# Kernel optimization log

Hardware: AMD Instinct MI355X
Metric: run time of the kernel (lower is better)

## Reference

```python
import jax, jax.numpy as jnp
import numpy as np

B, D, H = 65536, 32, 128


def setup_inputs() -> dict:
    key = jax.random.key(0)
    ks = jax.random.split(key, 6)
    return {
        "x": jax.random.normal(ks[0], (B, 1, D), dtype=jnp.float32),
        "W1": jax.random.normal(ks[1], (D, H), dtype=jnp.float32) * (1.0 / np.sqrt(D)),
        "b1": jax.random.normal(ks[2], (H,), dtype=jnp.float32) * 0.01,
        "W2": jax.random.normal(ks[3], (H, D), dtype=jnp.float32) * (1.0 / np.sqrt(H)),
        "b2": jax.random.normal(ks[4], (D,), dtype=jnp.float32) * 0.01,
        "theta_0": jnp.array([0.5], dtype=jnp.float32),
    }


def reference(x, W1, b1, W2, b2, theta_0):
    # x: (B, 1, D). Network u: D -> H -> D with tanh (transformation=none, no bounds).
    xf = x[:, 0, :]  # (B, D)

    def u_fn(xv):  # (D,) -> (D,)
        h = jnp.tanh(xv @ W1 + b1)
        return h @ W2 + b2

    # div u = trace of per-sample Jacobian, computed in ONE vectorized forward-mode
    # sweep (replaces the per-dimension torch.autograd.grad loop).
    div_u = jax.vmap(lambda xv: jnp.trace(jax.jacfwd(u_fn)(xv)))(xf)  # (B,)

    u_x = jax.vmap(u_fn)(xf)  # (B, D)
    grad_log_pi = -xf  # standard normal: grad log pi(x) = -x, shape (B, D)
    grad_log_pi_u = jnp.sum(grad_log_pi * u_x, axis=-1)  # (B,)  == (B,1,D)@(B,D,1) flattened

    out = (grad_log_pi_u + div_u + theta_0)[:, None]  # (B, 1)
    return out
```

## Files before the change

### kernel.cpp

```cpp
#include <hip/hip_runtime.h>


#define NROWS 65536
#define DD 32
#define HH 128
#define NTILE 25

typedef __attribute__((ext_vector_type(8))) short short8;
typedef __attribute__((ext_vector_type(4))) float f32x4;

static __device__ __forceinline__ unsigned short f2bf(float f) {
    unsigned u = __float_as_uint(f);
    u += 0x7fff + ((u >> 16) & 1);
    return (unsigned short)(u >> 16);
}
static __device__ __forceinline__ float bf2f(unsigned short h) {
    return __uint_as_float(((unsigned)h) << 16);
}

__global__ __launch_bounds__(256) void stein_pack(
    const float* __restrict__ W1, const float* __restrict__ W2,
    const float* __restrict__ b2, unsigned short* __restrict__ packed,
    float* __restrict__ c) {
    const int blk = blockIdx.x;
    if (blk < NTILE) {
        for (int idx = threadIdx.x; idx < 512; idx += 256) {
            const int l = idx >> 3, j = idx & 7;
            const int k = (l >> 4) * 8 + j;
            const int cc = l & 15;
            unsigned short val;
            if (blk < 8) {
                val = f2bf(W1[k * HH + blk * 16 + cc]);
            } else if (blk < 16) {
                float w = W1[k * HH + (blk - 8) * 16 + cc];
                val = f2bf(w - bf2f(f2bf(w)));
            } else {
                const int n = (blk - 16) * 16 + cc;
                float w = (n < HH) ? W2[n * DD + k] : ((n == HH) ? b2[k] : 0.f);
                val = f2bf(w);
            }
            packed[blk * 512 + idx] = val;
        }
    } else {
        const int k = threadIdx.x;
        if (k < HH) {
            float acc = 0.f;
#pragma unroll
            for (int i = 0; i < DD; ++i)
                acc = fmaf(W1[i * HH + k], W2[k * DD + i], acc);
            c[k] = acc;
        }
    }
}

__global__ __launch_bounds__(256) void stein_main(
    const float* __restrict__ x, const float* __restrict__ b1,
    const float* __restrict__ theta, const unsigned short* __restrict__ packed,
    const float* __restrict__ c, float* __restrict__ out) {
    __shared__ unsigned short lb[NTILE * 512];

    {
        const float4* src = (const float4*)packed;
        float4* dst = (float4*)lb;
        for (int i = threadIdx.x; i < NTILE * 512 / 8; i += 256) dst[i] = src[i];
    }
    __syncthreads();

    const int lane = threadIdx.x & 63;
    const int wv = threadIdx.x >> 6;
    const int quad = lane >> 4;
    const int cl = lane & 15;
    const int rowbase = blockIdx.x * 64 + wv * 16;

    const float* xr = x + (size_t)(rowbase + cl) * DD + quad * 8;
    const float4 x0 = *(const float4*)xr;
    const float4 x1 = *(const float4*)(xr + 4);
    const float xv[8] = {x0.x, x0.y, x0.z, x0.w, x1.x, x1.y, x1.z, x1.w};
    short8 aHi, aLo;
#pragma unroll
    for (int j = 0; j < 8; ++j) {
        const unsigned short h = f2bf(xv[j]);
        aHi[j] = (short)h;
        aLo[j] = (short)f2bf(xv[j] - bf2f(h));
    }

    float ckv[8], b1v[8];
#pragma unroll
    for (int t = 0; t < 8; ++t) {
        ckv[t] = c[t * 16 + cl];
        b1v[t] = b1[t * 16 + cl];
    }

    const f32x4 zero = {0.f, 0.f, 0.f, 0.f};
    float sa[4] = {0.f, 0.f, 0.f, 0.f};

#pragma unroll
    for (int t = 0; t < 8; ++t) {
        const short8 bH = *(const short8*)(lb + t * 512 + lane * 8);
        const short8 bL = *(const short8*)(lb + (8 + t) * 512 + lane * 8);
        const short8 bW = *(const short8*)(lb + (16 + t) * 512 + lane * 8);
        f32x4 z = zero;
        z = __builtin_amdgcn_mfma_f32_16x16x32_bf16(aLo, bH, z, 0, 0, 0);
        z = __builtin_amdgcn_mfma_f32_16x16x32_bf16(aHi, bL, z, 0, 0, 0);
        z = __builtin_amdgcn_mfma_f32_16x16x32_bf16(aHi, bH, z, 0, 0, 0);
        const f32x4 v = __builtin_amdgcn_mfma_f32_16x16x32_bf16(aHi, bW, zero, 0, 0, 0);
#pragma unroll
        for (int r = 0; r < 4; ++r) {
            float zz = z[r] + b1v[t];
            zz = fminf(fmaxf(zz, -15.f), 15.f);
            const float e = __expf(2.f * zz);
            const float h = fmaf(-2.f, __builtin_amdgcn_rcpf(e + 1.f), 1.f);
            const float ck = ckv[t];
            sa[r] += ck - h * fmaf(h, ck, v[r]);
        }
    }
    {
        const short8 bW = *(const short8*)(lb + 24 * 512 + lane * 8);
        const f32x4 v = __builtin_amdgcn_mfma_f32_16x16x32_bf16(aHi, bW, zero, 0, 0, 0);
#pragma unroll
        for (int r = 0; r < 4; ++r) sa[r] -= v[r];
    }

#pragma unroll
    for (int r = 0; r < 4; ++r) {
#pragma unroll
        for (int m = 1; m < 16; m <<= 1) sa[r] += __shfl_xor(sa[r], m, 64);
    }

    if (cl == 0) {
        const float th = theta[0];
        float4 o;
        o.x = sa[0] + th;
        o.y = sa[1] + th;
        o.z = sa[2] + th;
        o.w = sa[3] + th;
        *(float4*)(out + rowbase + quad * 4) = o;
    }
}

extern "C" void kernel_launch(void* const* d_in, const int* in_sizes, int n_in,
                              void* d_out, int out_size, void* d_ws, size_t ws_size,
                              hipStream_t stream) {
    const float* x = (const float*)d_in[0];
    const float* W1 = (const float*)d_in[1];
    const float* b1 = (const float*)d_in[2];
    const float* W2 = (const float*)d_in[3];
    const float* b2 = (const float*)d_in[4];
    const float* theta = (const float*)d_in[5];
    float* out = (float*)d_out;

    unsigned short* packed = (unsigned short*)d_ws;
    float* c = (float*)((char*)d_ws + NTILE * 512 * 2);

    stein_pack<<<NTILE + 1, 256, 0, stream>>>(W1, W2, b2, packed, c);
    stein_main<<<NROWS / 64, 256, 0, stream>>>(x, b1, theta, packed, c, out);
}
```

Baseline: 73.51 us.

## Fuse weight packing into main kernel and process 128 rows per block

Removes the separate packing kernel and its workspace round trip. Each block now converts W1, W2 and b2 to split-bf16 tiles in shared memory and computes the W1·W2 diagonal itself, using 512 threads that each cover 16 rows per wave. It also drops the tanh input clamp and moves c and b1 from registers to shared-memory reads. In exchange, every block repeats the weight conversion from L2, and relying on exp overflowing to inf without the clamp is a small numerical risk.

```diff
diff --git a/kernel.cpp b/kernel.cpp
--- a/kernel.cpp
+++ b/kernel.cpp
@@ -18,63 +18,84 @@
     return __uint_as_float(((unsigned)h) << 16);
 }
 
-__global__ __launch_bounds__(256) void stein_pack(
-    const float* __restrict__ W1, const float* __restrict__ W2,
-    const float* __restrict__ b2, unsigned short* __restrict__ packed,
-    float* __restrict__ c) {
-    const int blk = blockIdx.x;
-    if (blk < NTILE) {
-        for (int idx = threadIdx.x; idx < 512; idx += 256) {
-            const int l = idx >> 3, j = idx & 7;
-            const int k = (l >> 4) * 8 + j;
-            const int cc = l & 15;
-            unsigned short val;
-            if (blk < 8) {
-                val = f2bf(W1[k * HH + blk * 16 + cc]);
-            } else if (blk < 16) {
-                float w = W1[k * HH + (blk - 8) * 16 + cc];
-                val = f2bf(w - bf2f(f2bf(w)));
-            } else {
-                const int n = (blk - 16) * 16 + cc;
-                float w = (n < HH) ? W2[n * DD + k] : ((n == HH) ? b2[k] : 0.f);
-                val = f2bf(w);
-            }
-            packed[blk * 512 + idx] = val;
-        }
-    } else {
-        const int k = threadIdx.x;
-        if (k < HH) {
-            float acc = 0.f;
-#pragma unroll
-            for (int i = 0; i < DD; ++i)
-                acc = fmaf(W1[i * HH + k], W2[k * DD + i], acc);
-            c[k] = acc;
-        }
-    }
-}
+__global__ __launch_bounds__(512, 4) void stein_fused(
+    const float* __restrict__ x, const float* __restrict__ W1,
+    const float* __restrict__ b1, const float* __restrict__ W2,
+    const float* __restrict__ b2, const float* __restrict__ theta,
+    float* __restrict__ out) {
+    __shared__ unsigned short lb[NTILE * 512];
+    __shared__ float cs[HH];
+    __shared__ float b1s[HH];
 
-__global__ __launch_bounds__(256) void stein_main(
-    const float* __restrict__ x, const float* __restrict__ b1,
-    const float* __restrict__ theta, const unsigned short* __restrict__ packed,
-    const float* __restrict__ c, float* __restrict__ out) {
-    __shared__ unsigned short lb[NTILE * 512];
-
-    {
-        const float4* src = (const float4*)packed;
-        float4* dst = (float4*)lb;
-        for (int i = threadIdx.x; i < NTILE * 512 / 8; i += 256) dst[i] = src[i];
-    }
-    __syncthreads();
-
-    const int lane = threadIdx.x & 63;
-    const int wv = threadIdx.x >> 6;
+    const int tid = threadIdx.x;
+    const int lane = tid & 63;
+    const int wv = tid >> 6;
     const int quad = lane >> 4;
     const int cl = lane & 15;
-    const int rowbase = blockIdx.x * 64 + wv * 16;
+    const int rowbase = blockIdx.x * 128 + wv * 16;
 
     const float* xr = x + (size_t)(rowbase + cl) * DD + quad * 8;
     const float4 x0 = *(const float4*)xr;
     const float4 x1 = *(const float4*)(xr + 4);
+
+    if (tid < 256) {
+        const int n = tid & 127;
+        const int half = tid >> 7;
+        const int t = n >> 4, cc = n & 15;
+#pragma unroll
+        for (int g = 0; g < 2; ++g) {
+            const int kg = half * 2 + g;
+            short8 hi, lo;
+#pragma unroll
+            for (int j = 0; j < 8; ++j) {
+                const float w = W1[(kg * 8 + j) * HH + n];
+                const unsigned short h = f2bf(w);
+                hi[j] = (short)h;
+                lo[j] = (short)f2bf(w - bf2f(h));
+            }
+            *(short8*)(lb + t * 512 + (kg * 16 + cc) * 8) = hi;
+            *(short8*)(lb + (8 + t) * 512 + (kg * 16 + cc) * 8) = lo;
+        }
+    } else if (tid < 384) {
+        const int n = tid - 256;
+        const int t2 = 16 + (n >> 4), cc = n & 15;
+        float row[32];
+        const float4* wr = (const float4*)(W2 + n * DD);
+#pragma unroll
+        for (int q = 0; q < 8; ++q) {
+            const float4 f = wr[q];
+            row[4 * q + 0] = f.x;
+            row[4 * q + 1] = f.y;
+            row[4 * q + 2] = f.z;
+            row[4 * q + 3] = f.w;
+        }
+        float acc = 0.f;
+#pragma unroll
+        for (int k = 0; k < 32; ++k) acc = fmaf(W1[k * HH + n], row[k], acc);
+        cs[n] = acc;
+#pragma unroll
+        for (int g = 0; g < 4; ++g) {
+            short8 v;
+#pragma unroll
+            for (int j = 0; j < 8; ++j) v[j] = (short)f2bf(row[g * 8 + j]);
+            *(short8*)(lb + t2 * 512 + (g * 16 + cc) * 8) = v;
+        }
+    } else {
+        const int u = tid - 384;
+        if (u < 16) {
+#pragma unroll
+            for (int g = 0; g < 4; ++g) {
+                short8 v;
+#pragma unroll
+                for (int j = 0; j < 8; ++j)
+                    v[j] = (u == 0) ? (short)f2bf(b2[g * 8 + j]) : (short)0;
+                *(short8*)(lb + 24 * 512 + (g * 16 + u) * 8) = v;
+            }
+        }
+        b1s[u] = b1[u];
+    }
+    __syncthreads();
+
     const float xv[8] = {x0.x, x0.y, x0.z, x0.w, x1.x, x1.y, x1.z, x1.w};
     short8 aHi, aLo;
 #pragma unroll
@@ -82,13 +103,6 @@
         const unsigned short h = f2bf(xv[j]);
         aHi[j] = (short)h;
         aLo[j] = (short)f2bf(xv[j] - bf2f(h));
-    }
-
-    float ckv[8], b1v[8];
-#pragma unroll
-    for (int t = 0; t < 8; ++t) {
-        ckv[t] = c[t * 16 + cl];
-        b1v[t] = b1[t * 16 + cl];
     }
 
     const f32x4 zero = {0.f, 0.f, 0.f, 0.f};
@@ -104,13 +118,13 @@
         z = __builtin_amdgcn_mfma_f32_16x16x32_bf16(aHi, bL, z, 0, 0, 0);
         z = __builtin_amdgcn_mfma_f32_16x16x32_bf16(aHi, bH, z, 0, 0, 0);
         const f32x4 v = __builtin_amdgcn_mfma_f32_16x16x32_bf16(aHi, bW, zero, 0, 0, 0);
+        const float ck = cs[t * 16 + cl];
+        const float bb = b1s[t * 16 + cl];
 #pragma unroll
         for (int r = 0; r < 4; ++r) {
-            float zz = z[r] + b1v[t];
-            zz = fminf(fmaxf(zz, -15.f), 15.f);
+            const float zz = z[r] + bb;
             const float e = __expf(2.f * zz);
             const float h = fmaf(-2.f, __builtin_amdgcn_rcpf(e + 1.f), 1.f);
-            const float ck = ckv[t];
             sa[r] += ck - h * fmaf(h, ck, v[r]);
         }
     }
@@ -149,9 +163,5 @@
     const float* theta = (const float*)d_in[5];
     float* out = (float*)d_out;
 
-    unsigned short* packed = (unsigned short*)d_ws;
-    float* c = (float*)((char*)d_ws + NTILE * 512 * 2);
-
-    stein_pack<<<NTILE + 1, 256, 0, stream>>>(W1, W2, b2, packed, c);
-    stein_main<<<NROWS / 64, 256, 0, stream>>>(x, b1, theta, packed, c, out);
+    stein_fused<<<NROWS / 128, 512, 0, stream>>>(x, W1, b1, W2, b2, theta, out);
 }
```

Result: faster. 72.03 us (-2.0%).

## Read packed weights directly from global/L2 instead of staging in LDS

Applied to the files above, without the earlier changes.

Drops the per-block LDS staging of the packed bf16 weight tiles and the __syncthreads, so each wave reads B-fragments straight from global memory, where the small table should stay cache-resident. It also shrinks blocks to 128 threads with a launch-bounds occupancy hint, packs c and b1 into one float2 table, and replaces the clamped __expf with a raw exp2 intrinsic. The aim is to remove the per-block copy of roughly 25 KB and the barrier stall. The cost is repeated global/L2 loads per wave and possible overflow handling differences in tanh for large inputs, though exp2 overflowing to inf still gives h=1.

```diff
diff --git a/kernel.cpp b/kernel.cpp
--- a/kernel.cpp
+++ b/kernel.cpp
@@ -20,8 +20,8 @@
 
 __global__ __launch_bounds__(256) void stein_pack(
     const float* __restrict__ W1, const float* __restrict__ W2,
-    const float* __restrict__ b2, unsigned short* __restrict__ packed,
-    float* __restrict__ c) {
+    const float* __restrict__ b1, const float* __restrict__ b2,
+    unsigned short* __restrict__ packed, float2* __restrict__ cb) {
     const int blk = blockIdx.x;
     if (blk < NTILE) {
         for (int idx = threadIdx.x; idx < 512; idx += 256) {
@@ -32,11 +32,12 @@
             if (blk < 8) {
                 val = f2bf(W1[k * HH + blk * 16 + cc]);
             } else if (blk < 16) {
-                float w = W1[k * HH + (blk - 8) * 16 + cc];
+                const float w = W1[k * HH + (blk - 8) * 16 + cc];
                 val = f2bf(w - bf2f(f2bf(w)));
             } else {
                 const int n = (blk - 16) * 16 + cc;
-                float w = (n < HH) ? W2[n * DD + k] : ((n == HH) ? b2[k] : 0.f);
+                const float w = (n < HH) ? W2[n * DD + k]
+                                         : ((n == HH) ? b2[k] : 0.f);
                 val = f2bf(w);
             }
             packed[blk * 512 + idx] = val;
@@ -48,29 +49,21 @@
 #pragma unroll
             for (int i = 0; i < DD; ++i)
                 acc = fmaf(W1[i * HH + k], W2[k * DD + i], acc);
-            c[k] = acc;
+            cb[k] = make_float2(acc, b1[k]);
         }
     }
 }
 
-__global__ __launch_bounds__(256) void stein_main(
-    const float* __restrict__ x, const float* __restrict__ b1,
-    const float* __restrict__ theta, const unsigned short* __restrict__ packed,
-    const float* __restrict__ c, float* __restrict__ out) {
-    __shared__ unsigned short lb[NTILE * 512];
-
-    {
-        const float4* src = (const float4*)packed;
-        float4* dst = (float4*)lb;
-        for (int i = threadIdx.x; i < NTILE * 512 / 8; i += 256) dst[i] = src[i];
-    }
-    __syncthreads();
-
-    const int lane = threadIdx.x & 63;
-    const int wv = threadIdx.x >> 6;
+__global__ __launch_bounds__(128, 6) void stein_main(
+    const float* __restrict__ x, const float* __restrict__ theta,
+    const unsigned short* __restrict__ packed, const float2* __restrict__ cb,
+    float* __restrict__ out) {
+    const int tid = threadIdx.x;
+    const int lane = tid & 63;
+    const int wv = tid >> 6;
     const int quad = lane >> 4;
     const int cl = lane & 15;
-    const int rowbase = blockIdx.x * 64 + wv * 16;
+    const int rowbase = blockIdx.x * 32 + wv * 16;
 
     const float* xr = x + (size_t)(rowbase + cl) * DD + quad * 8;
     const float4 x0 = *(const float4*)xr;
@@ -84,21 +77,16 @@
         aLo[j] = (short)f2bf(xv[j] - bf2f(h));
     }
 
-    float ckv[8], b1v[8];
-#pragma unroll
-    for (int t = 0; t < 8; ++t) {
-        ckv[t] = c[t * 16 + cl];
-        b1v[t] = b1[t * 16 + cl];
-    }
-
     const f32x4 zero = {0.f, 0.f, 0.f, 0.f};
     float sa[4] = {0.f, 0.f, 0.f, 0.f};
+    const float C2LOG2E = 2.8853900817779268f;
 
 #pragma unroll
     for (int t = 0; t < 8; ++t) {
-        const short8 bH = *(const short8*)(lb + t * 512 + lane * 8);
-        const short8 bL = *(const short8*)(lb + (8 + t) * 512 + lane * 8);
-        const short8 bW = *(const short8*)(lb + (16 + t) * 512 + lane * 8);
+        const short8 bH = *(const short8*)(packed + t * 512 + lane * 8);
+        const short8 bL = *(const short8*)(packed + (8 + t) * 512 + lane * 8);
+        const short8 bW = *(const short8*)(packed + (16 + t) * 512 + lane * 8);
+        const float2 cbv = cb[t * 16 + cl];
         f32x4 z = zero;
         z = __builtin_amdgcn_mfma_f32_16x16x32_bf16(aLo, bH, z, 0, 0, 0);
         z = __builtin_amdgcn_mfma_f32_16x16x32_bf16(aHi, bL, z, 0, 0, 0);
@@ -106,16 +94,14 @@
         const f32x4 v = __builtin_amdgcn_mfma_f32_16x16x32_bf16(aHi, bW, zero, 0, 0, 0);
 #pragma unroll
         for (int r = 0; r < 4; ++r) {
-            float zz = z[r] + b1v[t];
-            zz = fminf(fmaxf(zz, -15.f), 15.f);
-            const float e = __expf(2.f * zz);
+            const float zz = z[r] + cbv.y;
+            const float e = __builtin_amdgcn_exp2f(zz * C2LOG2E);
             const float h = fmaf(-2.f, __builtin_amdgcn_rcpf(e + 1.f), 1.f);
-            const float ck = ckv[t];
-            sa[r] += ck - h * fmaf(h, ck, v[r]);
+            sa[r] += cbv.x - h * fmaf(h, cbv.x, v[r]);
         }
     }
     {
-        const short8 bW = *(const short8*)(lb + 24 * 512 + lane * 8);
+        const short8 bW = *(const short8*)(packed + 24 * 512 + lane * 8);
         const f32x4 v = __builtin_amdgcn_mfma_f32_16x16x32_bf16(aHi, bW, zero, 0, 0, 0);
 #pragma unroll
         for (int r = 0; r < 4; ++r) sa[r] -= v[r];
@@ -150,8 +136,8 @@
     float* out = (float*)d_out;
 
     unsigned short* packed = (unsigned short*)d_ws;
-    float* c = (float*)((char*)d_ws + NTILE * 512 * 2);
+    float2* cb = (float2*)((char*)d_ws + NTILE * 512 * 2);
 
-    stein_pack<<<NTILE + 1, 256, 0, stream>>>(W1, W2, b2, packed, c);
-    stein_main<<<NROWS / 64, 256, 0, stream>>>(x, b1, theta, packed, c, out);
+    stein_pack<<<NTILE + 1, 256, 0, stream>>>(W1, W2, b1, b2, packed, cb);
+    stein_main<<<NROWS / 32, 128, 0, stream>>>(x, theta, packed, cb, out);
 }
```

After: 76.85 us. 1.05x slower.
